# Optimization experiments

Hardware: AMD Instinct MI355X
Metric: run time of the kernel (lower is better)

Reference implementation:

```python
import jax, jax.numpy as jnp
import numpy as np

D_MODEL = 1024; D_STATE = 64; D_CONV = 4; EXPAND = 2; HEADDIM = 128; NGROUPS = 1; CHUNK = 256
D_INNER = EXPAND * D_MODEL            # 2048
NHEADS = D_INNER // HEADDIM           # 16
CONV_DIM = D_INNER + 2 * NGROUPS * D_STATE   # 2176
D_IN_PROJ = 2 * D_INNER + 2 * NGROUPS * D_STATE + NHEADS  # 4240
B = 4; G = 256; L = 2048
EPS = 1e-5


def setup_inputs() -> dict:
    key = jax.random.key(0)
    ks = jax.random.split(key, 12)
    def nrm(k, shape, s=0.02):
        return jax.random.normal(k, shape, jnp.float32) * s
    return dict(
        local_repr=jax.random.normal(ks[0], (B, L, D_MODEL), jnp.float32),
        global_repr=jax.random.normal(ks[1], (B, G, D_MODEL), jnp.float32),
        norm1_w=jnp.ones((D_MODEL,), jnp.float32), norm1_b=jnp.zeros((D_MODEL,), jnp.float32),
        norm2_w=jnp.ones((D_MODEL,), jnp.float32), norm2_b=jnp.zeros((D_MODEL,), jnp.float32),
        norm3_w=jnp.ones((D_MODEL,), jnp.float32), norm3_b=jnp.zeros((D_MODEL,), jnp.float32),
        in_proj_w=nrm(ks[2], (D_IN_PROJ, D_MODEL)),
        conv_w=nrm(ks[3], (CONV_DIM, D_CONV), 0.2),
        conv_b=jnp.zeros((CONV_DIM,), jnp.float32),
        dt_bias=jnp.log(jnp.expm1(jax.random.uniform(ks[4], (NHEADS,), jnp.float32, 1e-3, 0.1))),
        A_log=jnp.log(jax.random.uniform(ks[5], (NHEADS,), jnp.float32, 1.0, 16.0)),
        D_skip=jnp.ones((NHEADS,), jnp.float32),
        ssd_norm_w=jnp.ones((D_INNER,), jnp.float32),
        out_proj_w=nrm(ks[6], (D_MODEL, D_INNER)),
        ffn_w1=nrm(ks[7], (D_MODEL // 2, D_MODEL)),
        ffn_b1=jnp.zeros((D_MODEL // 2,), jnp.float32),
        ffn_w2=nrm(ks[8], (D_MODEL, D_MODEL // 2)),
        ffn_b2=jnp.zeros((D_MODEL,), jnp.float32),
    )


def _ln(x, w, b):
    mu = jnp.mean(x, axis=-1, keepdims=True)
    var = jnp.mean((x - mu) ** 2, axis=-1, keepdims=True)
    return (x - mu) * jax.lax.rsqrt(var + EPS) * w + b


def _segsum(a):
    # a: (..., T) -> (..., T, T) lower-triangular sums a[j+1..i]
    T = a.shape[-1]
    cs = jnp.cumsum(a, axis=-1)
    diff = cs[..., :, None] - cs[..., None, :]
    mask = jnp.tril(jnp.ones((T, T), bool))
    return jnp.where(mask, diff, -jnp.inf)


def _ssd(xdt, a_dt, Bh, Ch):
    # xdt: (b,t,h,p) = x*dt ; a_dt: (b,t,h) = dt*A ; Bh,Ch: (b,t,h,n)
    b, t, h, p = xdt.shape
    n = Bh.shape[-1]
    c = t // CHUNK
    X = xdt.reshape(b, c, CHUNK, h, p)
    Bc = Bh.reshape(b, c, CHUNK, h, n)
    Cc = Ch.reshape(b, c, CHUNK, h, n)
    Ac = a_dt.reshape(b, c, CHUNK, h).transpose(0, 3, 1, 2)  # (b,h,c,k)
    A_cum = jnp.cumsum(Ac, axis=-1)
    Lm = jnp.exp(_segsum(Ac))                                # (b,h,c,k,k)
    Y_diag = jnp.einsum('bckhn,bcshn,bhcks,bcshp->bckhp', Cc, Bc, Lm, X)
    decay_states = jnp.exp(A_cum[..., -1:] - A_cum)          # (b,h,c,k)
    states = jnp.einsum('bckhn,bhck,bckhp->bchpn', Bc, decay_states, X)
    A_last = jnp.pad(A_cum[..., -1], ((0, 0), (0, 0), (1, 0)))
    decay_chunk = jnp.exp(_segsum(A_last))                   # (b,h,c+1,c+1)
    states = jnp.concatenate([jnp.zeros_like(states[:, :1]), states], axis=1)
    new_states = jnp.einsum('bhzc,bchpn->bzhpn', decay_chunk, states)
    states_in = new_states[:, :-1]                           # (b,c,h,p,n)
    out_decay = jnp.exp(A_cum)                               # (b,h,c,k)
    Y_off = jnp.einsum('bckhn,bchpn,bhck->bckhp', Cc, states_in, out_decay)
    return (Y_diag + Y_off).reshape(b, t, h, p)


def _mamba2(x, in_proj_w, conv_w, conv_b, dt_bias, A_log, D_skip, ssd_norm_w, out_proj_w):
    b, t, _ = x.shape
    zxbcdt = x @ in_proj_w.T                                  # (b,t,D_IN_PROJ)
    z = zxbcdt[..., :D_INNER]
    xBC = zxbcdt[..., D_INNER:D_INNER + CONV_DIM]
    dt = jax.nn.softplus(zxbcdt[..., D_INNER + CONV_DIM:] + dt_bias)  # (b,t,h)
    # causal depthwise conv1d, kernel D_CONV
    xp = jnp.pad(xBC, ((0, 0), (D_CONV - 1, 0), (0, 0)))
    xBC = sum(xp[:, i:i + t, :] * conv_w[:, i] for i in range(D_CONV)) + conv_b
    xBC = jax.nn.silu(xBC)
    xs = xBC[..., :D_INNER].reshape(b, t, NHEADS, HEADDIM)
    Bm = xBC[..., D_INNER:D_INNER + NGROUPS * D_STATE].reshape(b, t, NGROUPS, D_STATE)
    Cm = xBC[..., D_INNER + NGROUPS * D_STATE:].reshape(b, t, NGROUPS, D_STATE)
    rep = NHEADS // NGROUPS
    Bh = jnp.repeat(Bm, rep, axis=2)
    Ch = jnp.repeat(Cm, rep, axis=2)
    A = -jnp.exp(A_log)                                       # (h,)
    Y = _ssd(xs * dt[..., None], dt * A, Bh, Ch)
    y = Y + D_skip[None, None, :, None] * xs
    y = y.reshape(b, t, D_INNER)
    # gated RMSNorm (norm_before_gate=False)
    y = y * jax.nn.silu(z)
    y = y * jax.lax.rsqrt(jnp.mean(y * y, axis=-1, keepdims=True) + EPS) * ssd_norm_w
    return y @ out_proj_w.T


def reference(local_repr, global_repr, norm1_w, norm1_b, norm2_w, norm2_b, norm3_w, norm3_b,
              in_proj_w, conv_w, conv_b, dt_bias, A_log, D_skip, ssd_norm_w, out_proj_w,
              ffn_w1, ffn_b1, ffn_w2, ffn_b2):
    local_n = _ln(local_repr, norm1_w, norm1_b)
    global_n = _ln(global_repr, norm2_w, norm2_b)
    x = jnp.concatenate([global_n, local_n], axis=1)          # (B, G+L, D)
    x = _mamba2(x, in_proj_w, conv_w, conv_b, dt_bias, A_log, D_skip, ssd_norm_w, out_proj_w)
    x = x[:, -local_n.shape[1]:, :] + local_n
    x = _ln(x, norm3_w, norm3_b)
    h = jax.nn.gelu(x @ ffn_w1.T + ffn_b1, approximate=False)
    return (h @ ffn_w2.T + ffn_b2) + x
```

## Files before the change

### kernel.cpp

```cpp
#include <hip/hip_runtime.h>
#include <math.h>

#define B_ 4
#define L_ 2048
#define G_ 256
#define T_ 2304
#define DM 1024
#define DINNER 2048
#define NH 16
#define HD 128
#define NSTATE 64
#define CONVD 2176
#define DPROJ 4240
#define NPROJ_PAD 4352
#define NCHUNK 9
#define CK 256
#define EPSV 1e-5f
#define CROWS 16

typedef unsigned short bf16t;
using bf16x8 = __attribute__((ext_vector_type(8))) short;
using f32x4  = __attribute__((ext_vector_type(4))) float;

__device__ __forceinline__ float bf2f(bf16t u) {
  return __uint_as_float(((unsigned int)u) << 16);
}
__device__ __forceinline__ bf16t f2bf(float f) {
  unsigned int u = __float_as_uint(f);
  u += 0x7FFFu + ((u >> 16) & 1u);
  return (bf16t)(u >> 16);
}

__device__ __forceinline__ void g2lds16(const bf16t* g, short* l) {
  __builtin_amdgcn_global_load_lds(
      (const __attribute__((address_space(1))) unsigned int*)g,
      (__attribute__((address_space(3))) unsigned int*)l, 16, 0, 0);
}

__device__ __forceinline__ float2 block_reduce2(float a, float b) {
  __shared__ float sa[4], sb[4];
  #pragma unroll
  for (int off = 32; off > 0; off >>= 1) {
    a += __shfl_down(a, off, 64);
    b += __shfl_down(b, off, 64);
  }
  int lane = threadIdx.x & 63, wid = threadIdx.x >> 6;
  if (lane == 0) { sa[wid] = a; sb[wid] = b; }
  __syncthreads();
  return make_float2(sa[0] + sa[1] + sa[2] + sa[3], sb[0] + sb[1] + sb[2] + sb[3]);
}

__global__ __launch_bounds__(256) void ln_cvt_kernel(
    const float* __restrict__ localr, const float* __restrict__ globalr,
    const float* __restrict__ w1, const float* __restrict__ b1,
    const float* __restrict__ w2, const float* __restrict__ b2,
    bf16t* __restrict__ x, const float* __restrict__ inpw,
    bf16t* __restrict__ inpw_bf) {
  int blk = blockIdx.x;
  if (blk < B_ * T_) {
    int t = blk % T_, b = blk / T_;
    const float *src, *w, *bb;
    if (t < G_) { src = globalr + ((long)b * G_ + t) * DM;        w = w2; bb = b2; }
    else        { src = localr  + ((long)b * L_ + (t - G_)) * DM; w = w1; bb = b1; }
    int d = threadIdx.x * 4;
    float4 v = *(const float4*)&src[d];
    float s = v.x + v.y + v.z + v.w;
    float sq = v.x * v.x + v.y * v.y + v.z * v.z + v.w * v.w;
    float2 r2 = block_reduce2(s, sq);
    float mu = r2.x * (1.f / DM);
    float var = r2.y * (1.f / DM) - mu * mu;
    float rstd = rsqrtf(var + EPSV);
    float4 wv = *(const float4*)&w[d];
    float4 bv = *(const float4*)&bb[d];
    ushort4 o;
    o.x = f2bf((v.x - mu) * rstd * wv.x + bv.x);
    o.y = f2bf((v.y - mu) * rstd * wv.y + bv.y);
    o.z = f2bf((v.z - mu) * rstd * wv.z + bv.z);
    o.w = f2bf((v.w - mu) * rstd * wv.w + bv.w);
    *(ushort4*)&x[(long)blk * DM + d] = o;
  } else {
    long i = (long)(blk - B_ * T_) * 1024 + threadIdx.x * 4;
    const long nreal = (long)DPROJ * DM, ntot = (long)NPROJ_PAD * DM;
    if (i < ntot) {
      ushort4 o = {0, 0, 0, 0};
      if (i < nreal) {
        float4 v = *(const float4*)&inpw[i];
        o.x = f2bf(v.x); o.y = f2bf(v.y); o.z = f2bf(v.z); o.w = f2bf(v.w);
      }
      *(ushort4*)&inpw_bf[i] = o;
    }
  }
}

__global__ __launch_bounds__(512) void gemm_inproj_mfma(
    const bf16t* __restrict__ A, const bf16t* __restrict__ W,
    bf16t* __restrict__ z, bf16t* __restrict__ xpre, float* __restrict__ dtr) {
  const int K = DM;
  __shared__ __align__(16) short LDS[128 * 136];
  short* As = LDS;
  short* Ws = LDS + 4096;
  int tid = threadIdx.x;
  int lane = tid & 63, w = tid >> 6;
  int wr = w >> 2, wc = w & 3;
  int bm = blockIdx.y * 128, bn = blockIdx.x * 256;

  const bf16t* gA  = A + (long)(bm + (tid >> 2)) * K + (tid & 3) * 8;
  const bf16t* gW1 = W + (long)(bn + (tid >> 2)) * K + (tid & 3) * 8;
  const bf16t* gW2 = W + (long)(bn + 128 + (tid >> 2)) * K + (tid & 3) * 8;
  short* lA  = As + tid * 8;
  short* lW1 = Ws + tid * 8;
  short* lW2 = Ws + (tid + 512) * 8;

  int arow = wr * 64 + (lane & 15);
  int brow = wc * 64 + (lane & 15);
  int koff = (lane >> 4) * 8;

  f32x4 acc[4][4] = {};
  for (int k0 = 0; k0 < K; k0 += 32) {
    g2lds16(gA + k0, lA);
    g2lds16(gW1 + k0, lW1);
    g2lds16(gW2 + k0, lW2);
    __syncthreads();
    bf16x8 af[4], bf[4];
    #pragma unroll
    for (int mi = 0; mi < 4; mi++) af[mi] = *(bf16x8*)&As[(arow + mi * 16) * 32 + koff];
    #pragma unroll
    for (int ni = 0; ni < 4; ni++) bf[ni] = *(bf16x8*)&Ws[(brow + ni * 16) * 32 + koff];
    #pragma unroll
    for (int mi = 0; mi < 4; mi++)
      #pragma unroll
      for (int ni = 0; ni < 4; ni++)
        acc[mi][ni] = __builtin_amdgcn_mfma_f32_16x16x32_bf16(af[mi], bf[ni], acc[mi][ni], 0, 0, 0);
    __syncthreads();
  }

  int rb = wr * 64 + (lane >> 4) * 4;
  if (bn == 4096 && wc == 2) {
    #pragma unroll
    for (int mi = 0; mi < 4; mi++)
      #pragma unroll
      for (int r = 0; r < 4; r++)
        dtr[(long)(bm + rb + mi * 16 + r) * NH + (lane & 15)] = acc[mi][0][r];
  }

  bf16t* Cs = (bf16t*)LDS;
  int cbh = (wc & 1) * 64 + (lane & 15);
  #pragma unroll
  for (int nh = 0; nh < 2; nh++) {
    __syncthreads();
    if ((wc >> 1) == nh) {
      #pragma unroll
      for (int mi = 0; mi < 4; mi++)
        #pragma unroll
        for (int ni = 0; ni < 4; ni++)
          #pragma unroll
          for (int r = 0; r < 4; r++)
            Cs[(rb + mi * 16 + r) * 136 + cbh + ni * 16] = f2bf(acc[mi][ni][r]);
    }
    __syncthreads();
    #pragma unroll
    for (int pass = 0; pass < 4; pass++) {
      int row = pass * 32 + (tid >> 4);
      int col = (tid & 15) * 8;
      int gcol = bn + nh * 128 + col;
      bf16x8 vv = *(bf16x8*)&Cs[row * 136 + col];
      long grow = bm + row;
      if (gcol < DINNER)                 *(bf16x8*)&z[grow * DINNER + gcol] = vv;
      else if (gcol < DINNER + CONVD)    *(bf16x8*)&xpre[grow * CONVD + (gcol - DINNER)] = vv;
    }
  }
}

template<int EPI, bool OFFS>
__global__ __launch_bounds__(256) void gemm_mfma(
    const bf16t* __restrict__ A, const bf16t* __restrict__ W,
    const float* __restrict__ bias, const bf16t* __restrict__ res,
    float* __restrict__ Cf, bf16t* __restrict__ Cb, int N, int K) {
  __shared__ __align__(16) short LDS[128 * 136];
  short* As = LDS;
  short* Ws = LDS + 128 * 32;
  int tid = threadIdx.x;
  int lane = tid & 63, w = tid >> 6;
  int wr = w >> 1, wc = w & 1;
  int bm = blockIdx.y * 128, bn = blockIdx.x * 128;
  long bmA = OFFS ? ((long)(bm >> 11) * T_ + G_ + (bm & 2047)) : (long)bm;

  int r1 = tid >> 2,         s1 = (tid & 3) * 8;
  int r2 = (tid + 256) >> 2, s2 = ((tid + 256) & 3) * 8;
  const bf16t* gA1 = A + (bmA + r1) * K + s1;
  const bf16t* gA2 = A + (bmA + r2) * K + s2;
  const bf16t* gW1 = W + (long)(bn + r1) * K + s1;
  const bf16t* gW2 = W + (long)(bn + r2) * K + s2;
  short* lA1 = As + tid * 8;
  short* lA2 = As + (tid + 256) * 8;
  short* lW1 = Ws + tid * 8;
  short* lW2 = Ws + (tid + 256) * 8;

  int arow = wr * 64 + (lane & 15);
  int brow = wc * 64 + (lane & 15);
  int koff = (lane >> 4) * 8;

  f32x4 acc[4][4] = {};
  for (int k0 = 0; k0 < K; k0 += 32) {
    g2lds16(gA1 + k0, lA1);
    g2lds16(gA2 + k0, lA2);
    g2lds16(gW1 + k0, lW1);
    g2lds16(gW2 + k0, lW2);
    __syncthreads();
    bf16x8 af[4], bf[4];
    #pragma unroll
    for (int mi = 0; mi < 4; mi++) af[mi] = *(bf16x8*)&As[(arow + mi * 16) * 32 + koff];
    #pragma unroll
    for (int ni = 0; ni < 4; ni++) bf[ni] = *(bf16x8*)&Ws[(brow + ni * 16) * 32 + koff];
    #pragma unroll
    for (int mi = 0; mi < 4; mi++)
      #pragma unroll
      for (int ni = 0; ni < 4; ni++)
        acc[mi][ni] = __builtin_amdgcn_mfma_f32_16x16x32_bf16(af[mi], bf[ni], acc[mi][ni], 0, 0, 0);
    __syncthreads();
  }

  int rb = wr * 64 + (lane >> 4) * 4;
  int cb = wc * 64 + (lane & 15);

  if (EPI == 3) {
    float* Cs32 = (float*)LDS;
    #pragma unroll
    for (int pass = 0; pass < 2; pass++) {
      __syncthreads();
      if (wr == pass) {
        #pragma unroll
        for (int mi = 0; mi < 4; mi++)
          #pragma unroll
          for (int ni = 0; ni < 4; ni++)
            #pragma unroll
            for (int r = 0; r < 4; r++) {
              int lrow = (lane >> 4) * 4 + mi * 16 + r;
              Cs32[lrow * 136 + cb + ni * 16] = acc[mi][ni][r];
            }
      }
      __syncthreads();
      #pragma unroll
      for (int q = 0; q < 4; q++) {
        int row = q * 16 + (tid >> 4);
        int col = (tid & 15) * 8;
        long grow = bm + pass * 64 + row; int gcol = bn + col;
        float4 v0 = *(float4*)&Cs32[row * 136 + col];
        float4 v1 = *(float4*)&Cs32[row * 136 + col + 4];
        float4 b0 = *(const float4*)&bias[gcol];
        float4 b1 = *(const float4*)&bias[gcol + 4];
        bf16x8 rv = *(const bf16x8*)&res[grow * N + gcol];
        v0.x += b0.x + bf2f((bf16t)rv[0]); v0.y += b0.y + bf2f((bf16t)rv[1]);
        v0.z += b0.z + bf2f((bf16t)rv[2]); v0.w += b0.w + bf2f((bf16t)rv[3]);
        v1.x += b1.x + bf2f((bf16t)rv[4]); v1.y += b1.y + bf2f((bf16t)rv[5]);
        v1.z += b1.z + bf2f((bf16t)rv[6]); v1.w += b1.w + bf2f((bf16t)rv[7]);
        *(float4*)&Cf[grow * N + gcol] = v0;
        *(float4*)&Cf[grow * N + gcol + 4] = v1;
      }
    }
    return;
  }

  __syncthreads();
  bf16t* Cs = (bf16t*)LDS;
  #pragma unroll
  for (int mi = 0; mi < 4; mi++)
    #pragma unroll
    for (int ni = 0; ni < 4; ni++)
      #pragma unroll
      for (int r = 0; r < 4; r++) {
        float v = acc[mi][ni][r];
        if (EPI == 2) {
          v += bias[bn + cb + ni * 16];
          v = 0.5f * v * (1.f + erff(v * 0.70710678118f));
        }
        Cs[(rb + mi * 16 + r) * 136 + cb + ni * 16] = f2bf(v);
      }
  __syncthreads();
  #pragma unroll
  for (int pass = 0; pass < 8; pass++) {
    int row = pass * 16 + (tid >> 4);
    int col = (tid & 15) * 8;
    bf16x8 vv = *(bf16x8*)&Cs[row * 136 + col];
    *(bf16x8*)&Cb[(long)(bm + row) * N + bn + col] = vv;
  }
}

__global__ __launch_bounds__(256) void cumsum_kernel(
    const float* __restrict__ dtraw, const float* __restrict__ dt_bias,
    const float* __restrict__ A_log, float* __restrict__ dt,
    float* __restrict__ Acum) {
  int bid = blockIdx.x;
  int c = bid % NCHUNK; int hh = bid / NCHUNK;
  int h = hh % NH; int b = hh / NH;
  int k = threadIdx.x;
  float a = -__expf(A_log[h]);
  long t = (long)b * T_ + c * CK + k;
  float v0 = dtraw[t * NH + h] + dt_bias[h];
  float dtv = (v0 > 20.f) ? v0 : log1pf(__expf(v0));
  dt[t * NH + h] = dtv;
  float v = dtv * a;
  __shared__ float buf[2][CK];
  int cur = 0;
  buf[0][k] = v; __syncthreads();
  for (int off = 1; off < CK; off <<= 1) {
    float tv = buf[cur][k];
    if (k >= off) tv += buf[cur][k - off];
    buf[1 - cur][k] = tv; cur ^= 1; __syncthreads();
  }
  Acum[(long)bid * CK + k] = buf[cur][k];
}

__global__ __launch_bounds__(256) void conv_kernel(
    const bf16t* __restrict__ xpre, const float* __restrict__ cw,
    const float* __restrict__ cb, bf16t* __restrict__ out) {
  int gt = blockIdx.x * 256 + threadIdx.x;
  int cg = gt % 272; int rt = gt / 272;
  int c0 = cg * 8;
  long r0 = (long)rt * CROWS;
  int t0 = (int)(r0 % T_);

  float wreg[4][8];
  #pragma unroll
  for (int j = 0; j < 8; j++) {
    float4 wa = *(const float4*)&cw[(c0 + j) * 4];
    wreg[0][j] = wa.x; wreg[1][j] = wa.y; wreg[2][j] = wa.z; wreg[3][j] = wa.w;
  }
  float4 cb0 = *(const float4*)&cb[c0];
  float4 cb1 = *(const float4*)&cb[c0 + 4];
  float bias[8] = {cb0.x, cb0.y, cb0.z, cb0.w, cb1.x, cb1.y, cb1.z, cb1.w};

  bf16x8 win[4];
  #pragma unroll
  for (int i = 0; i < 3; i++) {
    if (t0 - 3 + i >= 0) win[i] = *(const bf16x8*)&xpre[(r0 - 3 + i) * CONVD + c0];
    else                 win[i] = bf16x8{0,0,0,0,0,0,0,0};
  }

  #pragma unroll
  for (int k = 0; k < CROWS; k++) {
    win[3] = *(const bf16x8*)&xpre[(r0 + k) * CONVD + c0];
    float acc[8];
    #pragma unroll
    for (int j = 0; j < 8; j++) acc[j] = bias[j];
    #pragma unroll
    for (int i = 0; i < 4; i++)
      #pragma unroll
      for (int j = 0; j < 8; j++)
        acc[j] += bf2f((bf16t)win[i][j]) * wreg[i][j];
    bf16x8 o;
    #pragma unroll
    for (int j = 0; j < 8; j++) {
      float s = acc[j] / (1.f + __expf(-acc[j]));
      o[j] = (short)f2bf(s);
    }
    *(bf16x8*)&out[(r0 + k) * CONVD + c0] = o;
    win[0] = win[1]; win[1] = win[2]; win[2] = win[3];
  }
}

__global__ __launch_bounds__(256) void chunk_states_kernel(
    const bf16t* __restrict__ xbc, const float* __restrict__ dt,
    const float* __restrict__ Acum, float* __restrict__ cs) {
  int bid = blockIdx.x;
  int h = bid & 15; int bc = bid >> 4;
  int c = bc & 7; int b = bc >> 3;
  int tid = threadIdx.x;
  int lane = tid & 63, w = tid >> 6;
  long tch = (long)b * T_ + c * CK;
  int acb = ((b * NH + h) * NCHUNK + c) * CK;
  float Alast = Acum[acb + CK - 1];

  __shared__ bf16t Xt[128][72];
  __shared__ bf16t Bt[64][72];
  __shared__ float wk[64];

  f32x4 acc[8] = {};
  for (int kb = 0; kb < 4; kb++) {
    int s0 = kb * 64;
    __syncthreads();
    if (tid < 64)
      wk[tid] = __expf(Alast - Acum[acb + s0 + tid]) * dt[(tch + s0 + tid) * NH + h];
    __syncthreads();
    for (int e = tid; e < 64 * 32; e += 256) {
      int s = e & 63, p4 = e >> 6;
      ushort4 u = *(const ushort4*)&xbc[(tch + s0 + s) * CONVD + h * HD + p4 * 4];
      float wv = wk[s];
      Xt[p4 * 4 + 0][s] = f2bf(bf2f(u.x) * wv);
      Xt[p4 * 4 + 1][s] = f2bf(bf2f(u.y) * wv);
      Xt[p4 * 4 + 2][s] = f2bf(bf2f(u.z) * wv);
      Xt[p4 * 4 + 3][s] = f2bf(bf2f(u.w) * wv);
    }
    for (int e = tid; e < 64 * 16; e += 256) {
      int s = e & 63, n4 = e >> 6;
      ushort4 u = *(const ushort4*)&xbc[(tch + s0 + s) * CONVD + DINNER + n4 * 4];
      Bt[n4 * 4 + 0][s] = u.x; Bt[n4 * 4 + 1][s] = u.y;
      Bt[n4 * 4 + 2][s] = u.z; Bt[n4 * 4 + 3][s] = u.w;
    }
    __syncthreads();
    #pragma unroll
    for (int ks = 0; ks < 2; ks++) {
      int koff = (lane >> 4) * 8 + ks * 32;
      bf16x8 bfr = *(bf16x8*)&Bt[w * 16 + (lane & 15)][koff];
      #pragma unroll
      for (int mi = 0; mi < 8; mi++) {
        bf16x8 af = *(bf16x8*)&Xt[mi * 16 + (lane & 15)][koff];
        acc[mi] = __builtin_amdgcn_mfma_f32_16x16x32_bf16(af, bfr, acc[mi], 0, 0, 0);
      }
    }
  }
  int cbid = (b * NCHUNK + c) * NH + h;
  float* out = cs + (long)cbid * HD * NSTATE;
  int n = w * 16 + (lane & 15);
  #pragma unroll
  for (int mi = 0; mi < 8; mi++) {
    #pragma unroll
    for (int r = 0; r < 4; r++) {
      int p = mi * 16 + (lane >> 4) * 4 + r;
      out[p * NSTATE + n] = acc[mi][r];
    }
  }
}

__global__ __launch_bounds__(256) void state_pass_kernel(
    float* __restrict__ cs, const float* __restrict__ Acum) {
  int bh = blockIdx.x;
  int b = bh / NH, h = bh % NH;
  int e0 = blockIdx.y * 1024 + threadIdx.x;
  for (int q = 0; q < 4; q++) {
    int e = e0 + q * 256;
    float s = 0.f;
    for (int c = 0; c < NCHUNK; c++) {
      long idx = ((long)(b * NCHUNK + c) * NH + h) * (HD * NSTATE) + e;
      if (c < NCHUNK - 1) {
        float tmp = cs[idx];
        cs[idx] = s;
        float g = __expf(Acum[((b * NH + h) * NCHUNK + c) * CK + CK - 1]);
        s = s * g + tmp;
      } else {
        cs[idx] = s;
      }
    }
  }
}

__global__ __launch_bounds__(256) void ssd_y_kernel(
    const bf16t* __restrict__ xbc, const float* __restrict__ dt,
    const float* __restrict__ Acum, const float* __restrict__ sin_,
    const float* __restrict__ Dskip, bf16t* __restrict__ Y) {
  int bid = blockIdx.x;
  int h = bid & 15; int bc = bid >> 4;
  int c = 1 + (bc & 7); int b = bc >> 3;
  int rt = blockIdx.y;
  int tid = threadIdx.x;
  int lane = tid & 63, w = tid >> 6;
  int wr = w >> 1, wc = w & 1;
  long tch = (long)b * T_ + c * CK;
  long tbase = tch + rt * 128;
  int acb = ((b * NH + h) * NCHUNK + c) * CK;

  __shared__ bf16t Cs[128][72];
  __shared__ bf16t Bs[64][72];
  __shared__ bf16t Xt[128][72];
  __shared__ bf16t Sm[128][72];
  __shared__ float Akl[128];
  __shared__ float Asl[64];
  __shared__ float dts[64];

  for (int e = tid; e < 128 * 8; e += 256) {
    int row = e >> 3, seg = (e & 7) * 8;
    *(bf16x8*)&Cs[row][seg] =
        *(const bf16x8*)&xbc[(tbase + row) * CONVD + DINNER + NSTATE + seg];
  }
  if (tid < 128) Akl[tid] = Acum[acb + rt * 128 + tid];

  f32x4 acc[4][4] = {};
  int nsb = 2 * (rt + 1);
  for (int sb = 0; sb < nsb; sb++) {
    int s0 = sb * 64;
    __syncthreads();
    if (tid < 64) {
      Asl[tid] = Acum[acb + s0 + tid];
      dts[tid] = dt[(tch + s0 + tid) * NH + h];
    }
    __syncthreads();
    for (int e = tid; e < 64 * 8; e += 256) {
      int row = e >> 3, seg = (e & 7) * 8;
      *(bf16x8*)&Bs[row][seg] =
          *(const bf16x8*)&xbc[(tch + s0 + row) * CONVD + DINNER + seg];
    }
    for (int e = tid; e < 64 * 32; e += 256) {
      int s = e & 63, p4 = e >> 6;
      ushort4 u = *(const ushort4*)&xbc[(tch + s0 + s) * CONVD + h * HD + p4 * 4];
      float dtv = dts[s];
      Xt[p4 * 4 + 0][s] = f2bf(bf2f(u.x) * dtv);
      Xt[p4 * 4 + 1][s] = f2bf(bf2f(u.y) * dtv);
      Xt[p4 * 4 + 2][s] = f2bf(bf2f(u.z) * dtv);
      Xt[p4 * 4 + 3][s] = f2bf(bf2f(u.w) * dtv);
    }
    __syncthreads();
    {
      f32x4 sacc[2][4] = {};
      int rw0 = w * 32;
      #pragma unroll
      for (int ks = 0; ks < 2; ks++) {
        int koff = (lane >> 4) * 8 + ks * 32;
        bf16x8 a0 = *(bf16x8*)&Cs[rw0 + (lane & 15)][koff];
        bf16x8 a1 = *(bf16x8*)&Cs[rw0 + 16 + (lane & 15)][koff];
        #pragma unroll
        for (int ni = 0; ni < 4; ni++) {
          bf16x8 bfr = *(bf16x8*)&Bs[ni * 16 + (lane & 15)][koff];
          sacc[0][ni] = __builtin_amdgcn_mfma_f32_16x16x32_bf16(a0, bfr, sacc[0][ni], 0, 0, 0);
          sacc[1][ni] = __builtin_amdgcn_mfma_f32_16x16x32_bf16(a1, bfr, sacc[1][ni], 0, 0, 0);
        }
      }
      #pragma unroll
      for (int mi = 0; mi < 2; mi++) {
        #pragma unroll
        for (int ni = 0; ni < 4; ni++) {
          #pragma unroll
          for (int r = 0; r < 4; r++) {
            int row = rw0 + mi * 16 + (lane >> 4) * 4 + r;
            int scol = ni * 16 + (lane & 15);
            int kglob = rt * 128 + row;
            int sglob = s0 + scol;
            float val = 0.f;
            if (sglob <= kglob) val = sacc[mi][ni][r] * __expf(Akl[row] - Asl[scol]);
            Sm[row][scol] = f2bf(val);
          }
        }
      }
    }
    __syncthreads();
    #pragma unroll
    for (int ks = 0; ks < 2; ks++) {
      int koff = (lane >> 4) * 8 + ks * 32;
      bf16x8 af[4], bfr[4];
      #pragma unroll
      for (int mi = 0; mi < 4; mi++) af[mi] = *(bf16x8*)&Sm[wr * 64 + mi * 16 + (lane & 15)][koff];
      #pragma unroll
      for (int ni = 0; ni < 4; ni++) bfr[ni] = *(bf16x8*)&Xt[wc * 64 + ni * 16 + (lane & 15)][koff];
      #pragma unroll
      for (int mi = 0; mi < 4; mi++)
        #pragma unroll
        for (int ni = 0; ni < 4; ni++)
          acc[mi][ni] = __builtin_amdgcn_mfma_f32_16x16x32_bf16(af[mi], bfr[ni], acc[mi][ni], 0, 0, 0);
    }
  }

  float ekr[16];
  #pragma unroll
  for (int mi = 0; mi < 4; mi++)
    #pragma unroll
    for (int r = 0; r < 4; r++)
      ekr[mi * 4 + r] = __expf(Akl[wr * 64 + mi * 16 + (lane >> 4) * 4 + r]);

  int cbid = (b * NCHUNK + c) * NH + h;
  const float* sinb = sin_ + (long)cbid * HD * NSTATE;
  #pragma unroll
  for (int ni = 0; ni < 4; ni++) {
    f32x4 offacc[4] = {};
    int p = wc * 64 + ni * 16 + (lane & 15);
    #pragma unroll
    for (int ks = 0; ks < 2; ks++) {
      int koff = (lane >> 4) * 8 + ks * 32;
      const float* srow = sinb + p * NSTATE + koff;
      float4 sa = *(const float4*)srow;
      float4 sbv = *(const float4*)(srow + 4);
      bf16x8 bfr;
      bfr[0] = (short)f2bf(sa.x);  bfr[1] = (short)f2bf(sa.y);
      bfr[2] = (short)f2bf(sa.z);  bfr[3] = (short)f2bf(sa.w);
      bfr[4] = (short)f2bf(sbv.x); bfr[5] = (short)f2bf(sbv.y);
      bfr[6] = (short)f2bf(sbv.z); bfr[7] = (short)f2bf(sbv.w);
      #pragma unroll
      for (int mi = 0; mi < 4; mi++) {
        bf16x8 af = *(bf16x8*)&Cs[wr * 64 + mi * 16 + (lane & 15)][koff];
        offacc[mi] = __builtin_amdgcn_mfma_f32_16x16x32_bf16(af, bfr, offacc[mi], 0, 0, 0);
      }
    }
    #pragma unroll
    for (int mi = 0; mi < 4; mi++)
      #pragma unroll
      for (int r = 0; r < 4; r++)
        acc[mi][ni][r] += ekr[mi * 4 + r] * offacc[mi][r];
  }

  float dsk = Dskip[h];
  #pragma unroll
  for (int mi = 0; mi < 4; mi++) {
    #pragma unroll
    for (int r = 0; r < 4; r++) {
      int row = wr * 64 + mi * 16 + (lane >> 4) * 4 + r;
      long t = tbase + row;
      #pragma unroll
      for (int ni = 0; ni < 4; ni++) {
        int p = wc * 64 + ni * 16 + (lane & 15);
        float xsv = bf2f(xbc[t * CONVD + h * HD + p]);
        Y[t * DINNER + h * HD + p] = f2bf(acc[mi][ni][r] + dsk * xsv);
      }
    }
  }
}

__global__ __launch_bounds__(256) void gate_rms_cvt_kernel(
    const bf16t* __restrict__ z, const float* __restrict__ nw,
    bf16t* __restrict__ Y,
    const float* __restrict__ outw, const float* __restrict__ f1w,
    const float* __restrict__ f2w, bf16t* __restrict__ o_out,
    bf16t* __restrict__ o_f1, bf16t* __restrict__ o_f2) {
  int blk = blockIdx.x;
  if (blk < B_ * L_) {
    long r = (long)(blk >> 11) * T_ + G_ + (blk & 2047);
    const bf16t* zrow = z + r * DINNER;
    bf16t* yrow = Y + r * DINNER;
    int tid = threadIdx.x;
    float v[8]; float sq = 0.f;
    #pragma unroll
    for (int i = 0; i < 4; i++) {
      int d = tid * 2 + 512 * i;
      ushort2 zu = *(const ushort2*)&zrow[d];
      ushort2 yu = *(const ushort2*)&yrow[d];
      float z0 = bf2f(zu.x), z1 = bf2f(zu.y);
      float y0 = bf2f(yu.x) * (z0 / (1.f + __expf(-z0)));
      float y1 = bf2f(yu.y) * (z1 / (1.f + __expf(-z1)));
      v[2 * i] = y0; v[2 * i + 1] = y1;
      sq += y0 * y0 + y1 * y1;
    }
    float2 r2 = block_reduce2(sq, 0.f);
    float rms = rsqrtf(r2.x * (1.f / DINNER) + EPSV);
    #pragma unroll
    for (int i = 0; i < 4; i++) {
      int d = tid * 2 + 512 * i;
      ushort2 o;
      o.x = f2bf(v[2 * i] * rms * nw[d]);
      o.y = f2bf(v[2 * i + 1] * rms * nw[d + 1]);
      *(ushort2*)&yrow[d] = o;
    }
  } else {
    long i = (long)(blk - B_ * L_) * 1024 + threadIdx.x * 4;
    const long n1 = (long)DM * DINNER;
    const long n2 = (long)(DM / 2) * DM;
    const float* src; bf16t* dst; long off;
    if (i < n1) { src = outw; dst = o_out; off = i; }
    else if (i < n1 + n2) { src = f1w; dst = o_f1; off = i - n1; }
    else { src = f2w; dst = o_f2; off = i - n1 - n2; }
    float4 v = *(const float4*)&src[off];
    ushort4 o;
    o.x = f2bf(v.x); o.y = f2bf(v.y); o.z = f2bf(v.z); o.w = f2bf(v.w);
    *(ushort4*)&dst[off] = o;
  }
}

__global__ __launch_bounds__(256) void res_ln3_kernel(
    const bf16t* __restrict__ mfull, const bf16t* __restrict__ x,
    const float* __restrict__ w3, const float* __restrict__ b3,
    bf16t* __restrict__ x2) {
  int rl = blockIdx.x;
  int tl = rl & 2047, b = rl >> 11;
  long rt = (long)b * T_ + G_ + tl;
  const bf16t* m = mfull + (long)rl * DM;
  const bf16t* xr = x + rt * DM;
  int tid = threadIdx.x;
  float v[4]; float s = 0.f, sq = 0.f;
  #pragma unroll
  for (int i = 0; i < 2; i++) {
    int d = tid * 2 + 512 * i;
    ushort2 mu2 = *(const ushort2*)&m[d];
    ushort2 xu2 = *(const ushort2*)&xr[d];
    float a0 = bf2f(mu2.x) + bf2f(xu2.x);
    float a1 = bf2f(mu2.y) + bf2f(xu2.y);
    v[2 * i] = a0; v[2 * i + 1] = a1;
    s += a0 + a1; sq += a0 * a0 + a1 * a1;
  }
  float2 r2 = block_reduce2(s, sq);
  float mu = r2.x * (1.f / DM);
  float var = r2.y * (1.f / DM) - mu * mu;
  float rstd = rsqrtf(var + EPSV);
  bf16t* dst = x2 + (long)rl * DM;
  #pragma unroll
  for (int i = 0; i < 2; i++) {
    int d = tid * 2 + 512 * i;
    ushort2 o;
    o.x = f2bf((v[2 * i] - mu) * rstd * w3[d] + b3[d]);
    o.y = f2bf((v[2 * i + 1] - mu) * rstd * w3[d + 1] + b3[d + 1]);
    *(ushort2*)&dst[d] = o;
  }
}

extern "C" void kernel_launch(void* const* d_in, const int* in_sizes, int n_in,
                              void* d_out, int out_size, void* d_ws, size_t ws_size,
                              hipStream_t stream) {
  const float* localr = (const float*)d_in[0];
  const float* globalr= (const float*)d_in[1];
  const float* n1w = (const float*)d_in[2];
  const float* n1b = (const float*)d_in[3];
  const float* n2w = (const float*)d_in[4];
  const float* n2b = (const float*)d_in[5];
  const float* n3w = (const float*)d_in[6];
  const float* n3b = (const float*)d_in[7];
  const float* inpw= (const float*)d_in[8];
  const float* convw=(const float*)d_in[9];
  const float* convb=(const float*)d_in[10];
  const float* dtb = (const float*)d_in[11];
  const float* alog= (const float*)d_in[12];
  const float* dskp= (const float*)d_in[13];
  const float* ssdw= (const float*)d_in[14];
  const float* outw= (const float*)d_in[15];
  const float* f1w = (const float*)d_in[16];
  const float* f1b = (const float*)d_in[17];
  const float* f2w = (const float*)d_in[18];
  const float* f2b = (const float*)d_in[19];

  char* ws = (char*)d_ws;
  bf16t* x     = (bf16t*)(ws + 0);
  bf16t* z     = (bf16t*)(ws + 18874368);
  bf16t* mfull = (bf16t*)(ws + 18874368);
  bf16t* xpre  = (bf16t*)(ws + 56623104);
  bf16t* Yb    = (bf16t*)(ws + 56623104);
  float* dtraw = (float*)(ws + 96731136);
  float* dt    = (float*)(ws + 97320960);
  float* Acum  = (float*)(ws + 97910784);
  bf16t* xbc   = (bf16t*)(ws + 98500608);
  bf16t* x2bf  = (bf16t*)(ws + 98500608);
  bf16t* hbuf  = (bf16t*)(ws + 115277824);
  bf16t* outw_bf = (bf16t*)(ws + 123666432);
  bf16t* f1w_bf  = (bf16t*)(ws + 127860736);
  bf16t* f2w_bf  = (bf16t*)(ws + 128909312);
  float* cs    = (float*)(ws + 138608640);
  bf16t* inpw_bf = (bf16t*)(ws + 138608640);

  ln_cvt_kernel<<<B_ * T_ + 4352, 256, 0, stream>>>(
      localr, globalr, n1w, n1b, n2w, n2b, x, inpw, inpw_bf);

  gemm_inproj_mfma<<<dim3(NPROJ_PAD / 256, (B_ * T_) / 128), 512, 0, stream>>>(
      x, inpw_bf, z, xpre, dtraw);

  cumsum_kernel<<<B_ * NH * NCHUNK, 256, 0, stream>>>(dtraw, dtb, alog, dt, Acum);

  conv_kernel<<<(B_ * T_ / CROWS) * 272 / 256, 256, 0, stream>>>(xpre, convw, convb, xbc);

  chunk_states_kernel<<<B_ * (NCHUNK - 1) * NH, 256, 0, stream>>>(xbc, dt, Acum, cs);

  state_pass_kernel<<<dim3(B_ * NH, 8), 256, 0, stream>>>(cs, Acum);

  ssd_y_kernel<<<dim3(B_ * (NCHUNK - 1) * NH, 2), 256, 0, stream>>>(
      xbc, dt, Acum, cs, dskp, Yb);

  gate_rms_cvt_kernel<<<B_ * L_ + 3072, 256, 0, stream>>>(
      z, ssdw, Yb, outw, f1w, f2w, outw_bf, f1w_bf, f2w_bf);

  gemm_mfma<1, true><<<dim3(DM / 128, (B_ * L_) / 128), 256, 0, stream>>>(
      Yb, outw_bf, nullptr, nullptr, nullptr, mfull, DM, DINNER);

  res_ln3_kernel<<<B_ * L_, 256, 0, stream>>>(mfull, x, n3w, n3b, x2bf);

  gemm_mfma<2, false><<<dim3((DM / 2) / 128, (B_ * L_) / 128), 256, 0, stream>>>(
      x2bf, f1w_bf, f1b, nullptr, nullptr, hbuf, DM / 2, DM);

  gemm_mfma<3, false><<<dim3(DM / 128, (B_ * L_) / 128), 256, 0, stream>>>(
      hbuf, f2w_bf, f2b, x2bf, (float*)d_out, nullptr, DM, DM / 2);
}
```

Measured before the change: 554.7 us.

## Swizzle LDS layout in shared GEMM and route in-proj through it with 128x128 tiles

Drops the dedicated 512-thread 128x256 in-proj GEMM and runs the in-proj through the generic 256-thread 128x128 gemm_mfma template under a new epilogue mode that writes z, xpre and dt_raw. The LDS layout of every GEMM gets an XOR swizzle on the k-offset, applied at both the global-to-LDS copy and the fragment read, to cut bank conflicts. Smaller tiles mean more blocks and more reloads of the A operand. The dt tile block now returns early after writing only 16 columns.

Result: faster. 533.2 us (-3.9%).

```diff
diff --git a/kernel.cpp b/kernel.cpp
--- a/kernel.cpp
+++ b/kernel.cpp
@@ -92,90 +92,13 @@
   }
 }
 
-__global__ __launch_bounds__(512) void gemm_inproj_mfma(
-    const bf16t* __restrict__ A, const bf16t* __restrict__ W,
-    bf16t* __restrict__ z, bf16t* __restrict__ xpre, float* __restrict__ dtr) {
-  const int K = DM;
-  __shared__ __align__(16) short LDS[128 * 136];
-  short* As = LDS;
-  short* Ws = LDS + 4096;
-  int tid = threadIdx.x;
-  int lane = tid & 63, w = tid >> 6;
-  int wr = w >> 2, wc = w & 3;
-  int bm = blockIdx.y * 128, bn = blockIdx.x * 256;
-
-  const bf16t* gA  = A + (long)(bm + (tid >> 2)) * K + (tid & 3) * 8;
-  const bf16t* gW1 = W + (long)(bn + (tid >> 2)) * K + (tid & 3) * 8;
-  const bf16t* gW2 = W + (long)(bn + 128 + (tid >> 2)) * K + (tid & 3) * 8;
-  short* lA  = As + tid * 8;
-  short* lW1 = Ws + tid * 8;
-  short* lW2 = Ws + (tid + 512) * 8;
-
-  int arow = wr * 64 + (lane & 15);
-  int brow = wc * 64 + (lane & 15);
-  int koff = (lane >> 4) * 8;
-
-  f32x4 acc[4][4] = {};
-  for (int k0 = 0; k0 < K; k0 += 32) {
-    g2lds16(gA + k0, lA);
-    g2lds16(gW1 + k0, lW1);
-    g2lds16(gW2 + k0, lW2);
-    __syncthreads();
-    bf16x8 af[4], bf[4];
-    #pragma unroll
-    for (int mi = 0; mi < 4; mi++) af[mi] = *(bf16x8*)&As[(arow + mi * 16) * 32 + koff];
-    #pragma unroll
-    for (int ni = 0; ni < 4; ni++) bf[ni] = *(bf16x8*)&Ws[(brow + ni * 16) * 32 + koff];
-    #pragma unroll
-    for (int mi = 0; mi < 4; mi++)
-      #pragma unroll
-      for (int ni = 0; ni < 4; ni++)
-        acc[mi][ni] = __builtin_amdgcn_mfma_f32_16x16x32_bf16(af[mi], bf[ni], acc[mi][ni], 0, 0, 0);
-    __syncthreads();
-  }
-
-  int rb = wr * 64 + (lane >> 4) * 4;
-  if (bn == 4096 && wc == 2) {
-    #pragma unroll
-    for (int mi = 0; mi < 4; mi++)
-      #pragma unroll
-      for (int r = 0; r < 4; r++)
-        dtr[(long)(bm + rb + mi * 16 + r) * NH + (lane & 15)] = acc[mi][0][r];
-  }
-
-  bf16t* Cs = (bf16t*)LDS;
-  int cbh = (wc & 1) * 64 + (lane & 15);
-  #pragma unroll
-  for (int nh = 0; nh < 2; nh++) {
-    __syncthreads();
-    if ((wc >> 1) == nh) {
-      #pragma unroll
-      for (int mi = 0; mi < 4; mi++)
-        #pragma unroll
-        for (int ni = 0; ni < 4; ni++)
-          #pragma unroll
-          for (int r = 0; r < 4; r++)
-            Cs[(rb + mi * 16 + r) * 136 + cbh + ni * 16] = f2bf(acc[mi][ni][r]);
-    }
-    __syncthreads();
-    #pragma unroll
-    for (int pass = 0; pass < 4; pass++) {
-      int row = pass * 32 + (tid >> 4);
-      int col = (tid & 15) * 8;
-      int gcol = bn + nh * 128 + col;
-      bf16x8 vv = *(bf16x8*)&Cs[row * 136 + col];
-      long grow = bm + row;
-      if (gcol < DINNER)                 *(bf16x8*)&z[grow * DINNER + gcol] = vv;
-      else if (gcol < DINNER + CONVD)    *(bf16x8*)&xpre[grow * CONVD + (gcol - DINNER)] = vv;
-    }
-  }
-}
-
 template<int EPI, bool OFFS>
 __global__ __launch_bounds__(256) void gemm_mfma(
     const bf16t* __restrict__ A, const bf16t* __restrict__ W,
     const float* __restrict__ bias, const bf16t* __restrict__ res,
-    float* __restrict__ Cf, bf16t* __restrict__ Cb, int N, int K) {
+    float* __restrict__ Cf, bf16t* __restrict__ Cb,
+    bf16t* __restrict__ z, bf16t* __restrict__ xpre, float* __restrict__ dtr,
+    int N, int K) {
   __shared__ __align__(16) short LDS[128 * 136];
   short* As = LDS;
   short* Ws = LDS + 128 * 32;
@@ -185,8 +108,8 @@
   int bm = blockIdx.y * 128, bn = blockIdx.x * 128;
   long bmA = OFFS ? ((long)(bm >> 11) * T_ + G_ + (bm & 2047)) : (long)bm;
 
-  int r1 = tid >> 2,         s1 = (tid & 3) * 8;
-  int r2 = (tid + 256) >> 2, s2 = ((tid + 256) & 3) * 8;
+  int r1 = tid >> 2,         s1 = (((tid & 3) ^ ((r1 >> 1) & 3))) * 8;
+  int r2 = (tid + 256) >> 2, s2 = (((tid & 3) ^ ((r2 >> 1) & 3))) * 8;
   const bf16t* gA1 = A + (bmA + r1) * K + s1;
   const bf16t* gA2 = A + (bmA + r2) * K + s2;
   const bf16t* gW1 = W + (long)(bn + r1) * K + s1;
@@ -198,7 +121,7 @@
 
   int arow = wr * 64 + (lane & 15);
   int brow = wc * 64 + (lane & 15);
-  int koff = (lane >> 4) * 8;
+  int koff = (((lane >> 4) ^ (((lane & 15) >> 1) & 3))) * 8;
 
   f32x4 acc[4][4] = {};
   for (int k0 = 0; k0 < K; k0 += 32) {
@@ -222,6 +145,20 @@
 
   int rb = wr * 64 + (lane >> 4) * 4;
   int cb = wc * 64 + (lane & 15);
+
+  if (EPI == 0 && bn >= DINNER + CONVD) {
+    #pragma unroll
+    for (int mi = 0; mi < 4; mi++)
+      #pragma unroll
+      for (int ni = 0; ni < 4; ni++)
+        #pragma unroll
+        for (int r = 0; r < 4; r++) {
+          int col = cb + ni * 16;
+          if (col < NH)
+            dtr[(long)(bm + rb + mi * 16 + r) * NH + col] = acc[mi][ni][r];
+        }
+    return;
+  }
 
   if (EPI == 3) {
     float* Cs32 = (float*)LDS;
@@ -282,7 +219,13 @@
     int row = pass * 16 + (tid >> 4);
     int col = (tid & 15) * 8;
     bf16x8 vv = *(bf16x8*)&Cs[row * 136 + col];
-    *(bf16x8*)&Cb[(long)(bm + row) * N + bn + col] = vv;
+    long grow = bm + row; int gcol = bn + col;
+    if (EPI == 0) {
+      if (bn < DINNER) *(bf16x8*)&z[grow * DINNER + gcol] = vv;
+      else             *(bf16x8*)&xpre[grow * CONVD + (gcol - DINNER)] = vv;
+    } else {
+      *(bf16x8*)&Cb[grow * N + gcol] = vv;
+    }
   }
 }
 
@@ -732,8 +675,8 @@
   ln_cvt_kernel<<<B_ * T_ + 4352, 256, 0, stream>>>(
       localr, globalr, n1w, n1b, n2w, n2b, x, inpw, inpw_bf);
 
-  gemm_inproj_mfma<<<dim3(NPROJ_PAD / 256, (B_ * T_) / 128), 512, 0, stream>>>(
-      x, inpw_bf, z, xpre, dtraw);
+  gemm_mfma<0, false><<<dim3(NPROJ_PAD / 128, (B_ * T_) / 128), 256, 0, stream>>>(
+      x, inpw_bf, nullptr, nullptr, nullptr, nullptr, z, xpre, dtraw, NPROJ_PAD, DM);
 
   cumsum_kernel<<<B_ * NH * NCHUNK, 256, 0, stream>>>(dtraw, dtb, alog, dt, Acum);
 
@@ -750,13 +693,16 @@
       z, ssdw, Yb, outw, f1w, f2w, outw_bf, f1w_bf, f2w_bf);
 
   gemm_mfma<1, true><<<dim3(DM / 128, (B_ * L_) / 128), 256, 0, stream>>>(
-      Yb, outw_bf, nullptr, nullptr, nullptr, mfull, DM, DINNER);
+      Yb, outw_bf, nullptr, nullptr, nullptr, mfull, nullptr, nullptr, nullptr,
+      DM, DINNER);
 
   res_ln3_kernel<<<B_ * L_, 256, 0, stream>>>(mfull, x, n3w, n3b, x2bf);
 
   gemm_mfma<2, false><<<dim3((DM / 2) / 128, (B_ * L_) / 128), 256, 0, stream>>>(
-      x2bf, f1w_bf, f1b, nullptr, nullptr, hbuf, DM / 2, DM);
+      x2bf, f1w_bf, f1b, nullptr, nullptr, hbuf, nullptr, nullptr, nullptr,
+      DM / 2, DM);
 
   gemm_mfma<3, false><<<dim3(DM / 128, (B_ * L_) / 128), 256, 0, stream>>>(
-      hbuf, f2w_bf, f2b, x2bf, (float*)d_out, nullptr, DM, DM / 2);
-}
+      hbuf, f2w_bf, f2b, x2bf, (float*)d_out, nullptr, nullptr, nullptr, nullptr,
+      DM, DM / 2);
+}
```
